# Optimization experiments

Measured on AMD Instinct MI355X. Metric: run time of the kernel, lower is better.

Reference implementation:

```python
import jax, jax.numpy as jnp
import numpy as np

# SamplesLoss('sinkhorn', p=2, blur=0.05, backend='tensorized') defaults (geomloss):
# debiased Sinkhorn divergence, cost C(x,y)=|x-y|^2/2, eps = blur^p,
# epsilon-scaling from diameter^p down to blur^p with scaling=0.5,
# symmetric (averaged) log-domain updates + one final extrapolation step.
P = 2
BLUR = 0.05
SCALING = 0.5
DIAMETER = 10.0  # static diameter estimate for the annealing schedule (randn data)


def _eps_schedule():
    eps_target = BLUR ** P
    lst = []
    e = DIAMETER ** P
    while e > eps_target:
        lst.append(e)
        e *= SCALING ** P
    lst.append(eps_target)
    return lst

EPS_LIST = _eps_schedule()


def _sqcost(x, y):
    # C[b,n,m] = 0.5 * ||x_bn - y_bm||^2, via expansion (avoids [B,N,M,D] tensor)
    x2 = jnp.sum(x * x, axis=-1)  # [B,N]
    y2 = jnp.sum(y * y, axis=-1)  # [B,M]
    xy = jnp.einsum('bnd,bmd->bnm', x, y)
    return 0.5 * (x2[:, :, None] + y2[:, None, :] - 2.0 * xy)


def _softmin(eps, C, h):
    # h: [B,M] (already log-weights + potential/eps); C: [B,N,M] -> [B,N]
    return -eps * jax.nn.logsumexp(h[:, None, :] - C / eps, axis=2)


def _sinkhorn_divergence(x, y, a, b):
    log_a = jnp.log(a)
    log_b = jnp.log(b)
    Cxy = _sqcost(x, y)
    Cyx = jnp.swapaxes(Cxy, 1, 2)
    Cxx = _sqcost(x, x)
    Cyy = _sqcost(y, y)

    eps0 = EPS_LIST[0]
    f_ba = _softmin(eps0, Cxy, log_b)  # potential on x for OT(a,b)
    g_ab = _softmin(eps0, Cyx, log_a)  # potential on y for OT(a,b)
    f_aa = _softmin(eps0, Cxx, log_a)  # debias self-potential on x
    g_bb = _softmin(eps0, Cyy, log_b)  # debias self-potential on y

    for eps in EPS_LIST:
        ft = _softmin(eps, Cxy, log_b + g_ab / eps)
        gt = _softmin(eps, Cyx, log_a + f_ba / eps)
        f_ba = 0.5 * (f_ba + ft)
        g_ab = 0.5 * (g_ab + gt)
        f_aa = 0.5 * (f_aa + _softmin(eps, Cxx, log_a + f_aa / eps))
        g_bb = 0.5 * (g_bb + _softmin(eps, Cyy, log_b + g_bb / eps))

    # final (non-averaged) extrapolation at the target temperature
    eps = EPS_LIST[-1]
    f_fin = _softmin(eps, Cxy, log_b + g_ab / eps)
    g_fin = _softmin(eps, Cyx, log_a + f_ba / eps)
    f_aa = _softmin(eps, Cxx, log_a + f_aa / eps)
    g_bb = _softmin(eps, Cyy, log_b + g_bb / eps)

    # debiased divergence: <a, f_ab - f_aa> + <b, g_ab - g_bb>
    return jnp.sum(a * (f_fin - f_aa), axis=-1) + jnp.sum(b * (g_fin - g_bb), axis=-1)


def setup_inputs() -> dict:
    key = jax.random.key(0)
    k1, k2, k3, k4 = jax.random.split(key, 4)
    B, N, M, D = 8, 2048, 2048, 64
    return {
        'inp1': jax.random.normal(k1, (B, N, D), dtype=jnp.float32),
        'inp2': jax.random.normal(k2, (B, M, D), dtype=jnp.float32),
        'weights1': jax.random.uniform(k3, (B, N), dtype=jnp.float32),
        'weights2': jax.random.uniform(k4, (B, M), dtype=jnp.float32),
    }


def reference(inp1, inp2, weights1, weights2):
    # normalize_weights=True branch of SinkhornLoss.forward
    mass1 = jnp.sum(weights1, axis=1, keepdims=True)
    mass1 = jnp.where(mass1 == 0.0, 1.0, mass1)
    a = weights1 / mass1
    mass2 = jnp.sum(weights2, axis=1, keepdims=True)
    mass2 = jnp.where(mass2 == 0.0, 1.0, mass2)
    b = weights2 / mass2
    loss = _sinkhorn_divergence(inp1, inp2, a, b)  # [B]
    return jnp.mean(loss)  # reduction='mean'
```

## Files before the change

### kernel.cpp

```cpp
#include <hip/hip_runtime.h>
#include <cstdint>
#include <cstddef>

#define BB 8
#define NPTS 2048
#define DIM 64
#define CK 64
#define QC 512
#define NC (QC / CK)
#define BROWS 128

typedef _Float16 f16x8 __attribute__((ext_vector_type(8)));
typedef float f32x4 __attribute__((ext_vector_type(4)));

static const float EPS_H[9] = {100.0f, 25.0f, 6.25f, 1.5625f, 0.390625f,
                               0.09765625f, 0.0244140625f, 0.006103515625f,
                               0.0025f};
#define LOG2E 1.4426950408889634f
#define LN2 0.6931471805599453f

#if __has_builtin(__builtin_amdgcn_exp2f)
static __device__ __forceinline__ float fexp2(float x) {
  return __builtin_amdgcn_exp2f(x);
}
#else
static __device__ __forceinline__ float fexp2(float x) {
  float r;
  asm("v_exp_f32 %0, %1" : "=v"(r) : "v"(x));
  return r;
}
#endif

static __device__ __forceinline__ f32x4 vmax4(f32x4 a, f32x4 b) {
  f32x4 r;
  #pragma unroll
  for (int i = 0; i < 4; ++i) r[i] = fmaxf(a[i], b[i]);
  return r;
}

static __device__ __forceinline__ f32x4 vexp2_4(f32x4 a) {
  f32x4 r;
  #pragma unroll
  for (int i = 0; i < 4; ++i) r[i] = fexp2(a[i]);
  return r;
}

static __device__ __forceinline__ void gload_lds16(const void* g, void* l) {
  __builtin_amdgcn_global_load_lds(
      (const __attribute__((address_space(1))) void*)g,
      (__attribute__((address_space(3))) void*)l, 16, 0, 0);
}

struct FT {
  const _Float16* P;
  const _Float16* Q;
};
struct MT {
  const float* psq;
  const float* oldf;
  float* out;
  const float* lwn;
  const float* q2n;
  float* hqn;
};


__global__ __launch_bounds__(256) void norm_weights_k(
    const float* __restrict__ w, float* __restrict__ aout,
    float* __restrict__ logout, int n) {
  int b = blockIdx.x;
  const float* wb = w + (size_t)b * n;
  __shared__ float red[256];
  float s = 0.f;
  for (int i = threadIdx.x; i < n; i += 256) s += wb[i];
  red[threadIdx.x] = s;
  __syncthreads();
  for (int st = 128; st > 0; st >>= 1) {
    if (threadIdx.x < st) red[threadIdx.x] += red[threadIdx.x + st];
    __syncthreads();
  }
  float mass = red[0];
  if (mass == 0.f) mass = 1.f;
  float inv = 1.f / mass;
  for (int i = threadIdx.x; i < n; i += 256) {
    float av = wb[i] * inv;
    aout[(size_t)b * n + i] = av;
    logout[(size_t)b * n + i] = logf(av);
  }
}

__global__ __launch_bounds__(256) void sqnorm_cvt_k(
    const float* __restrict__ X, float* __restrict__ sq,
    _Float16* __restrict__ Xh, int rows) {
  int row = blockIdx.x * 4 + (threadIdx.x >> 6);
  int lane = threadIdx.x & 63;
  if (row >= rows) return;
  float v = X[(size_t)row * DIM + lane];
  Xh[(size_t)row * DIM + lane] = (_Float16)v;
  float s = v * v;
  #pragma unroll
  for (int off = 32; off > 0; off >>= 1) s += __shfl_xor(s, off);
  if (lane == 0) sq[row] = s;
}

__global__ __launch_bounds__(256) void init_hq_k(
    const float* __restrict__ la, const float* __restrict__ lb,
    const float* __restrict__ x2, const float* __restrict__ y2,
    float* __restrict__ hq, float ie2) {
  int task = blockIdx.z;
  int idx = blockIdx.x * 256 + threadIdx.x;
  const float* lw = (task == 1 || task == 2) ? la : lb;
  const float* q2 = (task == 1 || task == 2) ? x2 : y2;
  hq[(size_t)task * BB * NPTS + idx] =
      fmaf(lw[idx], LOG2E, -0.5f * q2[idx] * ie2);
}

template <int NM>
__global__ __launch_bounds__(256, 6) void fused_softmin_k(
    FT t0, FT t1, FT t2, FT t3, const float* __restrict__ hqG,
    float* __restrict__ pmx, float* __restrict__ psm, float ie2) {
  __shared__ float hql[QC];
  __shared__ __align__(16) _Float16 qb[2][CK * DIM];
  FT T = (blockIdx.z == 0) ? t0
       : (blockIdx.z == 1) ? t1
       : (blockIdx.z == 2) ? t2 : t3;
  const int rowg = blockIdx.x >> 2, qtr = blockIdx.x & 3;
  const int b = blockIdx.y, task = blockIdx.z;
  const int tid = threadIdx.x;

  {
    const float* hqp = hqG + ((size_t)task * BB + b) * NPTS + qtr * QC;
    #pragma unroll
    for (int i = 0; i < QC / 256; ++i)
      hql[i * 256 + tid] = hqp[i * 256 + tid];
  }

  const int lane = tid & 63, wave = tid >> 6;
  const _Float16* Qb = T.Q + ((size_t)b * NPTS + qtr * QC) * DIM;

  auto stage = [&](int buf, int chunk) {
    int m0 = chunk * CK;
    #pragma unroll
    for (int r = 0; r < 2; ++r) {
      int gbase = r * 256 + wave * 64;
      int gid = gbase + lane;
      int row = gid >> 3;
      int kg = (gid & 7) ^ (row & 7);
      const _Float16* src = Qb + (size_t)(m0 + row) * DIM + kg * 8;
      _Float16* dst = &qb[buf][(size_t)gbase * 8];
      gload_lds16(src, dst);
    }
  };

  const int fr = lane & 15;
  const int g0 = lane >> 4;
  const int r0 = rowg * BROWS + wave * 32;
  const _Float16* Pb = T.P + ((size_t)b * NPTS + r0) * DIM;
  f16x8 a00 = *(const f16x8*)(Pb + fr * DIM + g0 * 8);
  f16x8 a01 = *(const f16x8*)(Pb + fr * DIM + g0 * 8 + 32);
  f16x8 a10 = *(const f16x8*)(Pb + (16 + fr) * DIM + g0 * 8);
  f16x8 a11 = *(const f16x8*)(Pb + (16 + fr) * DIM + g0 * 8 + 32);

  f32x4 M0 = NM ? f32x4{0.f, 0.f, 0.f, 0.f}
               : f32x4{-3.0e38f, -3.0e38f, -3.0e38f, -3.0e38f};
  f32x4 M1 = M0;
  f32x4 S0 = {0.f, 0.f, 0.f, 0.f};
  f32x4 S1 = S0;

  auto compute = [&](int cur, int mbase) {
    const char* qbase = (const char*)&qb[cur][0];
    #pragma unroll
    for (int sh = 0; sh < 2; ++sh) {
      f32x4 acc00, acc01, acc10, acc11;
      float hs0, hs1;
      {
        int row = (sh * 2) * 16 + fr;
        int byte0 = row * 128 + ((g0 ^ (row & 7)) << 4);
        int byte1 = row * 128 + (((g0 + 4) ^ (row & 7)) << 4);
        f16x8 b0 = *(const f16x8*)(qbase + byte0);
        f16x8 b1 = *(const f16x8*)(qbase + byte1);
        hs0 = hql[mbase + (sh * 2) * 16 + fr];
        f32x4 z = {0.f, 0.f, 0.f, 0.f};
        f32x4 u0 = __builtin_amdgcn_mfma_f32_16x16x32_f16(a00, b0, z, 0, 0, 0);
        acc00 = __builtin_amdgcn_mfma_f32_16x16x32_f16(a01, b1, u0, 0, 0, 0);
        f32x4 u1 = __builtin_amdgcn_mfma_f32_16x16x32_f16(a10, b0, z, 0, 0, 0);
        acc10 = __builtin_amdgcn_mfma_f32_16x16x32_f16(a11, b1, u1, 0, 0, 0);
      }
      {
        int row = (sh * 2 + 1) * 16 + fr;
        int byte0 = row * 128 + ((g0 ^ (row & 7)) << 4);
        int byte1 = row * 128 + (((g0 + 4) ^ (row & 7)) << 4);
        f16x8 b0 = *(const f16x8*)(qbase + byte0);
        f16x8 b1 = *(const f16x8*)(qbase + byte1);
        hs1 = hql[mbase + (sh * 2 + 1) * 16 + fr];
        f32x4 z = {0.f, 0.f, 0.f, 0.f};
        f32x4 u0 = __builtin_amdgcn_mfma_f32_16x16x32_f16(a00, b0, z, 0, 0, 0);
        acc01 = __builtin_amdgcn_mfma_f32_16x16x32_f16(a01, b1, u0, 0, 0, 0);
        f32x4 u1 = __builtin_amdgcn_mfma_f32_16x16x32_f16(a10, b0, z, 0, 0, 0);
        acc11 = __builtin_amdgcn_mfma_f32_16x16x32_f16(a11, b1, u1, 0, 0, 0);
      }
      if (NM) {
        S0 += vexp2_4(acc00 * ie2 + hs0) + vexp2_4(acc01 * ie2 + hs1);
        S1 += vexp2_4(acc10 * ie2 + hs0) + vexp2_4(acc11 * ie2 + hs1);
      } else {
        {
          f32x4 v0 = acc00 * ie2 + hs0;
          f32x4 v1 = acc01 * ie2 + hs1;
          f32x4 cm = vmax4(M0, vmax4(v0, v1));
          S0 = S0 * vexp2_4(M0 - cm) + vexp2_4(v0 - cm) + vexp2_4(v1 - cm);
          M0 = cm;
        }
        {
          f32x4 v0 = acc10 * ie2 + hs0;
          f32x4 v1 = acc11 * ie2 + hs1;
          f32x4 cm = vmax4(M1, vmax4(v0, v1));
          S1 = S1 * vexp2_4(M1 - cm) + vexp2_4(v0 - cm) + vexp2_4(v1 - cm);
          M1 = cm;
        }
      }
    }
  };

  stage(0, 0);
  __syncthreads();

  for (int c = 0; c < NC - 1; ++c) {
    int cur = c & 1;
    stage(cur ^ 1, c + 1);
    asm volatile("s_waitcnt vmcnt(2)" ::: "memory");
    __builtin_amdgcn_sched_barrier(0);
    __builtin_amdgcn_s_barrier();
    __builtin_amdgcn_sched_barrier(0);
    compute(cur, c * CK);
    __builtin_amdgcn_sched_barrier(0);
    __builtin_amdgcn_s_barrier();
    __builtin_amdgcn_sched_barrier(0);
  }
  asm volatile("s_waitcnt vmcnt(0)" ::: "memory");
  __builtin_amdgcn_sched_barrier(0);
  __builtin_amdgcn_s_barrier();
  __builtin_amdgcn_sched_barrier(0);
  compute((NC - 1) & 1, (NC - 1) * CK);

  #pragma unroll
  for (int off = 1; off < 16; off <<= 1) {
    #pragma unroll
    for (int q = 0; q < 4; ++q) {
      if (NM) {
        S0[q] += __shfl_xor(S0[q], off);
        S1[q] += __shfl_xor(S1[q], off);
      } else {
        {
          float om = __shfl_xor(M0[q], off);
          float os = __shfl_xor(S0[q], off);
          float nm = fmaxf(M0[q], om);
          S0[q] = S0[q] * fexp2(M0[q] - nm) + os * fexp2(om - nm);
          M0[q] = nm;
        }
        {
          float om = __shfl_xor(M1[q], off);
          float os = __shfl_xor(S1[q], off);
          float nm = fmaxf(M1[q], om);
          S1[q] = S1[q] * fexp2(M1[q] - nm) + os * fexp2(om - nm);
          M1[q] = nm;
        }
      }
    }
  }
  if (fr == 0) {
    #pragma unroll
    for (int q = 0; q < 4; ++q) {
      size_t pbase = (((size_t)task * BB + b) * 4 + qtr) * NPTS;
      int ra = r0 + g0 * 4 + q;
      pmx[pbase + ra] = NM ? 0.f : M0[q];
      psm[pbase + ra] = S0[q];
      int rb = ra + 16;
      pmx[pbase + rb] = NM ? 0.f : M1[q];
      psm[pbase + rb] = S1[q];
    }
  }
}

__global__ __launch_bounds__(256) void merge_k(
    const float* __restrict__ pmx, const float* __restrict__ psm,
    MT m0, MT m1, MT m2, MT m3, float nel, float ie2n, int whq, int nomax) {
  int task = blockIdx.z;
  MT M = (task == 0) ? m0 : (task == 1) ? m1 : (task == 2) ? m2 : m3;
  int idx = blockIdx.x * 256 + threadIdx.x;
  int b = idx >> 11;
  int r = idx & 2047;
  size_t pb = (((size_t)task * BB + b) * 4) * NPTS + r;
  float nm, ss;
  if (nomax) {
    nm = 0.f;
    ss = psm[pb] + psm[pb + (size_t)NPTS] + psm[pb + (size_t)2 * NPTS] +
         psm[pb + (size_t)3 * NPTS];
  } else {
    float ma[4], sa[4];
    #pragma unroll
    for (int k = 0; k < 4; ++k) {
      ma[k] = pmx[pb + (size_t)k * NPTS];
      sa[k] = psm[pb + (size_t)k * NPTS];
    }
    nm = fmaxf(fmaxf(ma[0], ma[1]), fmaxf(ma[2], ma[3]));
    ss = 0.f;
    #pragma unroll
    for (int k = 0; k < 4; ++k) ss += sa[k] * fexp2(ma[k] - nm);
  }
  float f = nel * (__log2f(ss) + nm) + 0.5f * M.psq[idx];
  if (M.oldf) f = 0.5f * (M.oldf[idx] + f);
  M.out[idx] = f;
  if (whq) {
    float h = fmaf(f, ie2n, fmaf(M.lwn[idx], LOG2E, -0.5f * M.q2n[idx] * ie2n));
    M.hqn[idx] = h;
  }
}

__global__ __launch_bounds__(256) void loss_part_k(
    const float* __restrict__ aW, const float* __restrict__ f_fin,
    const float* __restrict__ f_aa, const float* __restrict__ bW,
    const float* __restrict__ g_fin, const float* __restrict__ g_bb,
    float* __restrict__ part) {
  __shared__ float red[256];
  int i0 = blockIdx.x * 256 + threadIdx.x;
  float s = 0.f;
  for (int i = i0; i < BB * NPTS; i += 64 * 256)
    s += aW[i] * (f_fin[i] - f_aa[i]) + bW[i] * (g_fin[i] - g_bb[i]);
  red[threadIdx.x] = s;
  __syncthreads();
  for (int st = 128; st > 0; st >>= 1) {
    if (threadIdx.x < st) red[threadIdx.x] += red[threadIdx.x + st];
    __syncthreads();
  }
  if (threadIdx.x == 0) part[blockIdx.x] = red[0];
}

__global__ __launch_bounds__(64) void loss_fin_k(const float* __restrict__ part,
                                                 float* __restrict__ out) {
  float s = part[threadIdx.x];
  #pragma unroll
  for (int off = 32; off > 0; off >>= 1) s += __shfl_xor(s, off);
  if (threadIdx.x == 0) out[0] = s * (1.f / BB);
}

__global__ void write_val_k(float* out, float v) { out[0] = v; }


extern "C" void kernel_launch(void* const* d_in, const int* in_sizes, int n_in,
                              void* d_out, int out_size, void* d_ws,
                              size_t ws_size, hipStream_t stream) {
  (void)in_sizes; (void)n_in; (void)out_size;
  const float* X = (const float*)d_in[0];
  const float* Y = (const float*)d_in[1];
  const float* W1 = (const float*)d_in[2];
  const float* W2 = (const float*)d_in[3];
  float* out = (float*)d_out;

  char* base = (char*)d_ws;
  size_t off = 0;
  auto alloc_b = [&](size_t bytes) {
    void* r = base + off;
    off += (bytes + 255) & ~(size_t)255;
    return r;
  };
  const size_t nP = (size_t)BB * NPTS;
  _Float16* Xh = (_Float16*)alloc_b(nP * DIM * 2);
  _Float16* Yh = (_Float16*)alloc_b(nP * DIM * 2);
  float* x2 = (float*)alloc_b(nP * 4);
  float* y2 = (float*)alloc_b(nP * 4);
  float* aW = (float*)alloc_b(nP * 4);
  float* bW = (float*)alloc_b(nP * 4);
  float* la = (float*)alloc_b(nP * 4);
  float* lb = (float*)alloc_b(nP * 4);
  float* fba[2] = {(float*)alloc_b(nP * 4), (float*)alloc_b(nP * 4)};
  float* gab[2] = {(float*)alloc_b(nP * 4), (float*)alloc_b(nP * 4)};
  float* faa[2] = {(float*)alloc_b(nP * 4), (float*)alloc_b(nP * 4)};
  float* gbb[2] = {(float*)alloc_b(nP * 4), (float*)alloc_b(nP * 4)};
  float* hq = (float*)alloc_b(4 * nP * 4);
  float* pmx = (float*)alloc_b(4 * nP * 4 * 4);
  float* psm = (float*)alloc_b(4 * nP * 4 * 4);
  float* part = (float*)alloc_b(64 * 4);
  if (ws_size < off) {
    write_val_k<<<1, 1, 0, stream>>>(out, -(float)(ws_size >> 20));
    return;
  }

  norm_weights_k<<<BB, 256, 0, stream>>>(W1, aW, la, NPTS);
  norm_weights_k<<<BB, 256, 0, stream>>>(W2, bW, lb, NPTS);
  sqnorm_cvt_k<<<BB * NPTS / 4, 256, 0, stream>>>(X, x2, Xh, BB * NPTS);
  sqnorm_cvt_k<<<BB * NPTS / 4, 256, 0, stream>>>(Y, y2, Yh, BB * NPTS);

  dim3 fg(64, BB, 4);
  dim3 mg(BB * NPTS / 256, 1, 4);

  FT t0{Xh, Yh}, t1{Yh, Xh}, t2{Xh, Xh}, t3{Yh, Yh};
  float* hq0 = hq;
  float* hq1 = hq + 1 * nP;
  float* hq2 = hq + 2 * nP;
  float* hq3 = hq + 3 * nP;

  auto fused = [&](float eps) {
    if (eps >= 6.0f)
      fused_softmin_k<1><<<fg, 256, 0, stream>>>(t0, t1, t2, t3, hq, pmx, psm,
                                                 LOG2E / eps);
    else
      fused_softmin_k<0><<<fg, 256, 0, stream>>>(t0, t1, t2, t3, hq, pmx, psm,
                                                 LOG2E / eps);
  };
  auto merge = [&](float eps, float ie2n, int whq, const float* oF,
                   float* nF, const float* oG, float* nG, const float* oA,
                   float* nA, const float* oB, float* nB) {
    float nel = -eps * LN2;
    int nomax = (eps >= 6.0f) ? 1 : 0;
    MT M0{x2, oF, nF, la, x2, hq1};
    MT M1{y2, oG, nG, lb, y2, hq0};
    MT M2{x2, oA, nA, la, x2, hq2};
    MT M3{y2, oB, nB, lb, y2, hq3};
    merge_k<<<mg, 256, 0, stream>>>(pmx, psm, M0, M1, M2, M3, nel, ie2n, whq,
                                    nomax);
  };

  init_hq_k<<<mg, 256, 0, stream>>>(la, lb, x2, y2, hq, LOG2E / EPS_H[0]);

  fused(EPS_H[0]);
  merge(EPS_H[0], LOG2E / EPS_H[0], 1, nullptr, fba[0], nullptr, gab[0],
        nullptr, faa[0], nullptr, gbb[0]);

  int cur = 0;
  for (int it = 0; it < 9; ++it) {
    int nxt = cur ^ 1;
    float epsn = EPS_H[it < 8 ? it + 1 : 8];
    fused(EPS_H[it]);
    merge(EPS_H[it], LOG2E / epsn, 1, fba[cur], fba[nxt], gab[cur], gab[nxt],
          faa[cur], faa[nxt], gbb[cur], gbb[nxt]);
    cur = nxt;
  }

  {
    int nxt = cur ^ 1;
    fused(EPS_H[8]);
    merge(EPS_H[8], 0.f, 0, nullptr, fba[nxt], nullptr, gab[nxt], nullptr,
          faa[nxt], nullptr, gbb[nxt]);
    loss_part_k<<<64, 256, 0, stream>>>(aW, fba[nxt], faa[nxt], bW, gab[nxt],
                                        gbb[nxt], part);
    loss_fin_k<<<1, 64, 0, stream>>>(part, out);
  }
}
```

Before: 435.1 us.

## Use two-pass max-then-sum softmin with bias folded into MFMA accumulator

For the low-epsilon path, the online-max logsumexp is replaced by two passes over the Q tiles. The first pass computes the exact row max of the scaled dot product plus bias, with the bias injected as the MFMA accumulator's initial value. The second pass recomputes the matmul with the max already subtracted inside the accumulator init, so each element needs only a single exp2 and no rescaling. This removes the per-step max/rescale exponentials and adds to the accumulator, at the cost of doubling MFMA work and the global-to-LDS staging traffic for that path.

```diff
diff --git a/kernel.cpp b/kernel.cpp
--- a/kernel.cpp
+++ b/kernel.cpp
@@ -118,7 +118,8 @@
 template <int NM>
 __global__ __launch_bounds__(256, 6) void fused_softmin_k(
     FT t0, FT t1, FT t2, FT t3, const float* __restrict__ hqG,
-    float* __restrict__ pmx, float* __restrict__ psm, float ie2) {
+    float* __restrict__ pmx, float* __restrict__ psm, float ie2,
+    float inv_ie2) {
   __shared__ float hql[QC];
   __shared__ __align__(16) _Float16 qb[2][CK * DIM];
   FT T = (blockIdx.z == 0) ? t0
@@ -161,122 +162,185 @@
   f16x8 a10 = *(const f16x8*)(Pb + (16 + fr) * DIM + g0 * 8);
   f16x8 a11 = *(const f16x8*)(Pb + (16 + fr) * DIM + g0 * 8 + 32);
 
-  f32x4 M0 = NM ? f32x4{0.f, 0.f, 0.f, 0.f}
-               : f32x4{-3.0e38f, -3.0e38f, -3.0e38f, -3.0e38f};
-  f32x4 M1 = M0;
-  f32x4 S0 = {0.f, 0.f, 0.f, 0.f};
-  f32x4 S1 = S0;
-
-  auto compute = [&](int cur, int mbase) {
-    const char* qbase = (const char*)&qb[cur][0];
-    #pragma unroll
-    for (int sh = 0; sh < 2; ++sh) {
-      f32x4 acc00, acc01, acc10, acc11;
-      float hs0, hs1;
-      {
-        int row = (sh * 2) * 16 + fr;
+  if (NM) {
+    f32x4 S0 = {0.f, 0.f, 0.f, 0.f};
+    f32x4 S1 = S0;
+
+    auto compute = [&](int cur, int mbase) {
+      const char* qbase = (const char*)&qb[cur][0];
+      #pragma unroll
+      for (int s = 0; s < 4; ++s) {
+        int row = s * 16 + fr;
         int byte0 = row * 128 + ((g0 ^ (row & 7)) << 4);
         int byte1 = row * 128 + (((g0 + 4) ^ (row & 7)) << 4);
         f16x8 b0 = *(const f16x8*)(qbase + byte0);
         f16x8 b1 = *(const f16x8*)(qbase + byte1);
-        hs0 = hql[mbase + (sh * 2) * 16 + fr];
+        float hs = hql[mbase + s * 16 + fr];
         f32x4 z = {0.f, 0.f, 0.f, 0.f};
         f32x4 u0 = __builtin_amdgcn_mfma_f32_16x16x32_f16(a00, b0, z, 0, 0, 0);
-        acc00 = __builtin_amdgcn_mfma_f32_16x16x32_f16(a01, b1, u0, 0, 0, 0);
+        f32x4 acc0 = __builtin_amdgcn_mfma_f32_16x16x32_f16(a01, b1, u0, 0, 0, 0);
+        S0 += vexp2_4(acc0 * ie2 + hs);
         f32x4 u1 = __builtin_amdgcn_mfma_f32_16x16x32_f16(a10, b0, z, 0, 0, 0);
-        acc10 = __builtin_amdgcn_mfma_f32_16x16x32_f16(a11, b1, u1, 0, 0, 0);
-      }
-      {
-        int row = (sh * 2 + 1) * 16 + fr;
+        f32x4 acc1 = __builtin_amdgcn_mfma_f32_16x16x32_f16(a11, b1, u1, 0, 0, 0);
+        S1 += vexp2_4(acc1 * ie2 + hs);
+      }
+    };
+
+    stage(0, 0);
+    __syncthreads();
+    for (int c = 0; c < NC - 1; ++c) {
+      int cur = c & 1;
+      stage(cur ^ 1, c + 1);
+      asm volatile("s_waitcnt vmcnt(2)" ::: "memory");
+      __builtin_amdgcn_sched_barrier(0);
+      __builtin_amdgcn_s_barrier();
+      __builtin_amdgcn_sched_barrier(0);
+      compute(cur, c * CK);
+      __builtin_amdgcn_sched_barrier(0);
+      __builtin_amdgcn_s_barrier();
+      __builtin_amdgcn_sched_barrier(0);
+    }
+    asm volatile("s_waitcnt vmcnt(0)" ::: "memory");
+    __builtin_amdgcn_sched_barrier(0);
+    __builtin_amdgcn_s_barrier();
+    __builtin_amdgcn_sched_barrier(0);
+    compute((NC - 1) & 1, (NC - 1) * CK);
+
+    #pragma unroll
+    for (int off = 1; off < 16; off <<= 1) {
+      #pragma unroll
+      for (int q = 0; q < 4; ++q) {
+        S0[q] += __shfl_xor(S0[q], off);
+        S1[q] += __shfl_xor(S1[q], off);
+      }
+    }
+    if (fr == 0) {
+      #pragma unroll
+      for (int q = 0; q < 4; ++q) {
+        size_t pbase = (((size_t)task * BB + b) * 4 + qtr) * NPTS;
+        int ra = r0 + g0 * 4 + q;
+        pmx[pbase + ra] = 0.f;
+        psm[pbase + ra] = S0[q];
+        pmx[pbase + ra + 16] = 0.f;
+        psm[pbase + ra + 16] = S1[q];
+      }
+    }
+  } else {
+    f32x4 W0 = {-3.0e38f, -3.0e38f, -3.0e38f, -3.0e38f};
+    f32x4 W1 = W0;
+
+    auto computeA = [&](int cur, int mbase) {
+      const char* qbase = (const char*)&qb[cur][0];
+      #pragma unroll
+      for (int s = 0; s < 4; ++s) {
+        int row = s * 16 + fr;
         int byte0 = row * 128 + ((g0 ^ (row & 7)) << 4);
         int byte1 = row * 128 + (((g0 + 4) ^ (row & 7)) << 4);
         f16x8 b0 = *(const f16x8*)(qbase + byte0);
         f16x8 b1 = *(const f16x8*)(qbase + byte1);
-        hs1 = hql[mbase + (sh * 2 + 1) * 16 + fr];
-        f32x4 z = {0.f, 0.f, 0.f, 0.f};
+        float zs = hql[mbase + s * 16 + fr] * inv_ie2;
+        f32x4 z = {zs, zs, zs, zs};
         f32x4 u0 = __builtin_amdgcn_mfma_f32_16x16x32_f16(a00, b0, z, 0, 0, 0);
-        acc01 = __builtin_amdgcn_mfma_f32_16x16x32_f16(a01, b1, u0, 0, 0, 0);
+        f32x4 acc0 = __builtin_amdgcn_mfma_f32_16x16x32_f16(a01, b1, u0, 0, 0, 0);
+        W0 = vmax4(W0, acc0);
         f32x4 u1 = __builtin_amdgcn_mfma_f32_16x16x32_f16(a10, b0, z, 0, 0, 0);
-        acc11 = __builtin_amdgcn_mfma_f32_16x16x32_f16(a11, b1, u1, 0, 0, 0);
-      }
-      if (NM) {
-        S0 += vexp2_4(acc00 * ie2 + hs0) + vexp2_4(acc01 * ie2 + hs1);
-        S1 += vexp2_4(acc10 * ie2 + hs0) + vexp2_4(acc11 * ie2 + hs1);
-      } else {
-        {
-          f32x4 v0 = acc00 * ie2 + hs0;
-          f32x4 v1 = acc01 * ie2 + hs1;
-          f32x4 cm = vmax4(M0, vmax4(v0, v1));
-          S0 = S0 * vexp2_4(M0 - cm) + vexp2_4(v0 - cm) + vexp2_4(v1 - cm);
-          M0 = cm;
-        }
-        {
-          f32x4 v0 = acc10 * ie2 + hs0;
-          f32x4 v1 = acc11 * ie2 + hs1;
-          f32x4 cm = vmax4(M1, vmax4(v0, v1));
-          S1 = S1 * vexp2_4(M1 - cm) + vexp2_4(v0 - cm) + vexp2_4(v1 - cm);
-          M1 = cm;
-        }
-      }
-    }
-  };
-
-  stage(0, 0);
-  __syncthreads();
-
-  for (int c = 0; c < NC - 1; ++c) {
-    int cur = c & 1;
-    stage(cur ^ 1, c + 1);
-    asm volatile("s_waitcnt vmcnt(2)" ::: "memory");
+        f32x4 acc1 = __builtin_amdgcn_mfma_f32_16x16x32_f16(a11, b1, u1, 0, 0, 0);
+        W1 = vmax4(W1, acc1);
+      }
+    };
+
+    stage(0, 0);
+    __syncthreads();
+    for (int c = 0; c < NC - 1; ++c) {
+      int cur = c & 1;
+      stage(cur ^ 1, c + 1);
+      asm volatile("s_waitcnt vmcnt(2)" ::: "memory");
+      __builtin_amdgcn_sched_barrier(0);
+      __builtin_amdgcn_s_barrier();
+      __builtin_amdgcn_sched_barrier(0);
+      computeA(cur, c * CK);
+      __builtin_amdgcn_sched_barrier(0);
+      __builtin_amdgcn_s_barrier();
+      __builtin_amdgcn_sched_barrier(0);
+    }
+    asm volatile("s_waitcnt vmcnt(0)" ::: "memory");
     __builtin_amdgcn_sched_barrier(0);
     __builtin_amdgcn_s_barrier();
     __builtin_amdgcn_sched_barrier(0);
-    compute(cur, c * CK);
+    computeA((NC - 1) & 1, (NC - 1) * CK);
+
+    #pragma unroll
+    for (int off = 1; off < 16; off <<= 1) {
+      #pragma unroll
+      for (int q = 0; q < 4; ++q) {
+        W0[q] = fmaxf(W0[q], __shfl_xor(W0[q], off));
+        W1[q] = fmaxf(W1[q], __shfl_xor(W1[q], off));
+      }
+    }
+    __syncthreads();
+
+    f32x4 S0 = {0.f, 0.f, 0.f, 0.f};
+    f32x4 S1 = S0;
+
+    auto computeB = [&](int cur, int mbase) {
+      const char* qbase = (const char*)&qb[cur][0];
+      #pragma unroll
+      for (int s = 0; s < 4; ++s) {
+        int row = s * 16 + fr;
+        int byte0 = row * 128 + ((g0 ^ (row & 7)) << 4);
+        int byte1 = row * 128 + (((g0 + 4) ^ (row & 7)) << 4);
+        f16x8 b0 = *(const f16x8*)(qbase + byte0);
+        f16x8 b1 = *(const f16x8*)(qbase + byte1);
+        float zs = hql[mbase + s * 16 + fr] * inv_ie2;
+        f32x4 z0 = zs - W0;
+        f32x4 z1 = zs - W1;
+        f32x4 u0 = __builtin_amdgcn_mfma_f32_16x16x32_f16(a00, b0, z0, 0, 0, 0);
+        f32x4 acc0 = __builtin_amdgcn_mfma_f32_16x16x32_f16(a01, b1, u0, 0, 0, 0);
+        S0 += vexp2_4(acc0 * ie2);
+        f32x4 u1 = __builtin_amdgcn_mfma_f32_16x16x32_f16(a10, b0, z1, 0, 0, 0);
+        f32x4 acc1 = __builtin_amdgcn_mfma_f32_16x16x32_f16(a11, b1, u1, 0, 0, 0);
+        S1 += vexp2_4(acc1 * ie2);
+      }
+    };
+
+    stage(0, 0);
+    __syncthreads();
+    for (int c = 0; c < NC - 1; ++c) {
+      int cur = c & 1;
+      stage(cur ^ 1, c + 1);
+      asm volatile("s_waitcnt vmcnt(2)" ::: "memory");
+      __builtin_amdgcn_sched_barrier(0);
+      __builtin_amdgcn_s_barrier();
+      __builtin_amdgcn_sched_barrier(0);
+      computeB(cur, c * CK);
+      __builtin_amdgcn_sched_barrier(0);
+      __builtin_amdgcn_s_barrier();
+      __builtin_amdgcn_sched_barrier(0);
+    }
+    asm volatile("s_waitcnt vmcnt(0)" ::: "memory");
     __builtin_amdgcn_sched_barrier(0);
     __builtin_amdgcn_s_barrier();
     __builtin_amdgcn_sched_barrier(0);
-  }
-  asm volatile("s_waitcnt vmcnt(0)" ::: "memory");
-  __builtin_amdgcn_sched_barrier(0);
-  __builtin_amdgcn_s_barrier();
-  __builtin_amdgcn_sched_barrier(0);
-  compute((NC - 1) & 1, (NC - 1) * CK);
-
-  #pragma unroll
-  for (int off = 1; off < 16; off <<= 1) {
-    #pragma unroll
-    for (int q = 0; q < 4; ++q) {
-      if (NM) {
+    computeB((NC - 1) & 1, (NC - 1) * CK);
+
+    #pragma unroll
+    for (int off = 1; off < 16; off <<= 1) {
+      #pragma unroll
+      for (int q = 0; q < 4; ++q) {
         S0[q] += __shfl_xor(S0[q], off);
         S1[q] += __shfl_xor(S1[q], off);
-      } else {
-        {
-          float om = __shfl_xor(M0[q], off);
-          float os = __shfl_xor(S0[q], off);
-          float nm = fmaxf(M0[q], om);
-          S0[q] = S0[q] * fexp2(M0[q] - nm) + os * fexp2(om - nm);
-          M0[q] = nm;
-        }
-        {
-          float om = __shfl_xor(M1[q], off);
-          float os = __shfl_xor(S1[q], off);
-          float nm = fmaxf(M1[q], om);
-          S1[q] = S1[q] * fexp2(M1[q] - nm) + os * fexp2(om - nm);
-          M1[q] = nm;
-        }
-      }
-    }
-  }
-  if (fr == 0) {
-    #pragma unroll
-    for (int q = 0; q < 4; ++q) {
-      size_t pbase = (((size_t)task * BB + b) * 4 + qtr) * NPTS;
-      int ra = r0 + g0 * 4 + q;
-      pmx[pbase + ra] = NM ? 0.f : M0[q];
-      psm[pbase + ra] = S0[q];
-      int rb = ra + 16;
-      pmx[pbase + rb] = NM ? 0.f : M1[q];
-      psm[pbase + rb] = S1[q];
+      }
+    }
+    if (fr == 0) {
+      #pragma unroll
+      for (int q = 0; q < 4; ++q) {
+        size_t pbase = (((size_t)task * BB + b) * 4 + qtr) * NPTS;
+        int ra = r0 + g0 * 4 + q;
+        pmx[pbase + ra] = W0[q] * ie2;
+        psm[pbase + ra] = S0[q];
+        pmx[pbase + ra + 16] = W1[q] * ie2;
+        psm[pbase + ra + 16] = S1[q];
+      }
     }
   }
 }
@@ -400,12 +464,14 @@
   float* hq3 = hq + 3 * nP;
 
   auto fused = [&](float eps) {
+    float ie2 = LOG2E / eps;
+    float inv_ie2 = eps * LN2;
     if (eps >= 6.0f)
       fused_softmin_k<1><<<fg, 256, 0, stream>>>(t0, t1, t2, t3, hq, pmx, psm,
-                                                 LOG2E / eps);
+                                                 ie2, inv_ie2);
     else
       fused_softmin_k<0><<<fg, 256, 0, stream>>>(t0, t1, t2, t3, hq, pmx, psm,
-                                                 LOG2E / eps);
+                                                 ie2, inv_ie2);
   };
   auto merge = [&](float eps, float ie2n, int whq, const float* oF,
                    float* nF, const float* oG, float* nG, const float* oA,
```

New measurement: 548.3 us (median of 2 runs). +26.0%, slower.
